# Kernel tuning notes

Measured on AMD Instinct MI355X. Metric: run time of the kernel, lower is better.

The kernel has to match this reference:

```python
import jax, jax.numpy as jnp
import numpy as np

NUM_NODES = 50000
NUM_GRAPHS = 64
HIDDEN = 256
F_IN = 256
NUM_EDGES = 800000


def setup_inputs() -> dict:
    key = jax.random.key(0)
    ks = jax.random.split(key, 8)
    x = jax.random.normal(ks[0], (NUM_NODES, F_IN), dtype=jnp.float32)
    edge_index = jax.random.randint(ks[1], (2, NUM_EDGES), 0, NUM_NODES, dtype=jnp.int64)
    batch = jnp.sort(jax.random.randint(ks[2], (NUM_NODES,), 0, NUM_GRAPHS, dtype=jnp.int64))
    # Glorot-ish init for weights, zeros for biases (as PyG GCNConv / Linear defaults)
    s1 = 1.0 / np.sqrt(F_IN)
    s2 = 1.0 / np.sqrt(HIDDEN)
    W1 = jax.random.uniform(ks[3], (F_IN, HIDDEN), jnp.float32, -s1, s1)
    b1 = jnp.zeros((HIDDEN,), jnp.float32)
    W2 = jax.random.uniform(ks[4], (HIDDEN, HIDDEN), jnp.float32, -s2, s2)
    b2 = jnp.zeros((HIDDEN,), jnp.float32)
    W_out = jax.random.uniform(ks[5], (HIDDEN, 1), jnp.float32, -s2, s2)
    b_out = jnp.zeros((1,), jnp.float32)
    return {"x": x, "edge_index": edge_index, "batch": batch,
            "W1": W1, "b1": b1, "W2": W2, "b2": b2,
            "W_out": W_out, "b_out": b_out}


def gcn_conv(x, W, b, src, dst, num_nodes):
    """GCNConv with added self-loops and symmetric D^{-1/2} A D^{-1/2} norm."""
    # degrees over edges incl. self-loops (src/dst already include them)
    deg = jax.ops.segment_sum(jnp.ones_like(src, dtype=x.dtype), dst,
                              num_segments=num_nodes)
    dinv = jax.lax.rsqrt(jnp.maximum(deg, 1e-12))
    norm = dinv[src] * dinv[dst]                       # [E+N]
    h = x @ W                                           # [N, H] dense GEMM
    msg = h[src] * norm[:, None]                        # gather + scale
    out = jax.ops.segment_sum(msg, dst, num_segments=num_nodes)  # scatter-add
    return out + b


def reference(x, edge_index, batch, W1, b1, W2, b2, W_out, b_out):
    n = x.shape[0]
    loops = jnp.arange(n, dtype=edge_index.dtype)
    src = jnp.concatenate([edge_index[0], loops])
    dst = jnp.concatenate([edge_index[1], loops])
    h = jax.nn.relu(gcn_conv(x, W1, b1, src, dst, n))
    h = jax.nn.relu(gcn_conv(h, W2, b2, src, dst, n))
    pooled = jax.ops.segment_sum(h, batch, num_segments=NUM_GRAPHS)  # [G, H]
    return pooled @ W_out + b_out
```

## Files before the change

kernel.cpp:

```cpp
#include <hip/hip_runtime.h>
#include <hip/hip_fp16.h>

#define N_NODES 50000
#define NFEAT   256
#define NGRAPH  64
#define NEDGE   800000
#define NBUCK   98
#define BWIN    16384

typedef __attribute__((ext_vector_type(8))) _Float16 half8;
typedef __attribute__((ext_vector_type(2))) _Float16 h2v;
typedef __attribute__((ext_vector_type(4))) float f32x4;
struct alignas(8) US4 { unsigned short x, y, z, w; };

static __device__ __forceinline__ float h2f(unsigned short u) {
    return __half2float(__ushort_as_half(u));
}
static __device__ __forceinline__ unsigned short f2h(float f) {
    return __half_as_ushort(__float2half(f));
}

__global__ __launch_bounds__(256) void k_bin(const int* __restrict__ src,
                                             const int* __restrict__ dst,
                                             int* __restrict__ bcnt,
                                             unsigned int* __restrict__ tmp) {
    __shared__ int hist[NBUCK];
    __shared__ int base[NBUCK];
    const int t = threadIdx.x;
    if (t < NBUCK) hist[t] = 0;
    __syncthreads();
    const int e0 = blockIdx.x * 1024 + t * 4;
    int s[4], d[4], b[4], rk[4];
#pragma unroll
    for (int i = 0; i < 4; ++i) {
        const int e = e0 + i;
        if (e < NEDGE) {
            s[i] = src[e];
            d[i] = dst[e];
            b[i] = d[i] >> 9;
            rk[i] = atomicAdd(&hist[b[i]], 1);
        } else {
            b[i] = -1;
        }
    }
    __syncthreads();
    if (t < NBUCK) base[t] = atomicAdd(&bcnt[t], hist[t]);
    __syncthreads();
#pragma unroll
    for (int i = 0; i < 4; ++i) {
        if (b[i] >= 0)
            tmp[(size_t)b[i] * BWIN + base[b[i]] + rk[i]] =
                ((unsigned int)s[i] << 16) | (unsigned int)d[i];
    }
}

__global__ void k_bscan(const int* __restrict__ bcnt, int* __restrict__ bbase) {
    const int l = threadIdx.x;
    const int i0 = 2 * l, i1 = 2 * l + 1;
    const int v0 = (i0 < NBUCK) ? bcnt[i0] : 0;
    const int v1 = (i1 < NBUCK) ? bcnt[i1] : 0;
    const int ps = v0 + v1;
    int incl = ps;
#pragma unroll
    for (int off = 1; off < 64; off <<= 1) {
        int u = __shfl_up(incl, off, 64);
        if (l >= off) incl += u;
    }
    const int excl = incl - ps;
    if (i0 < NBUCK) bbase[i0] = excl;
    if (i1 < NBUCK) bbase[i1] = excl + v0;
}

__global__ __launch_bounds__(256) void k_build(const unsigned int* __restrict__ tmp,
                                               const int* __restrict__ bcnt,
                                               const int* __restrict__ bbase,
                                               int* __restrict__ row_start,
                                               float* __restrict__ dinv,
                                               unsigned short* __restrict__ csr) {
    __shared__ int cnt[512];
    __shared__ int cur[512];
    __shared__ int wtot[4];
    const int bk = blockIdx.x, t = threadIdx.x;
    const int node0 = bk << 9;
    const int n = bcnt[bk];
    const unsigned int* rec = tmp + (size_t)bk * BWIN;
    cnt[t] = 0;
    cnt[t + 256] = 0;
    __syncthreads();
    for (int i = t; i < n; i += 256) atomicAdd(&cnt[rec[i] & 511], 1);
    __syncthreads();
    const int lane = t & 63, w = t >> 6;
    const int v0 = cnt[2 * t], v1 = cnt[2 * t + 1];
    const int ps = v0 + v1;
    int incl = ps;
#pragma unroll
    for (int off = 1; off < 64; off <<= 1) {
        int u = __shfl_up(incl, off, 64);
        if (lane >= off) incl += u;
    }
    if (lane == 63) wtot[w] = incl;
    __syncthreads();
    int wbase = 0;
#pragma unroll
    for (int k = 0; k < 4; ++k) wbase += (k < w) ? wtot[k] : 0;
    const int excl = wbase + incl - ps;
    const int gb = bbase[bk];
    const int g0 = node0 + 2 * t;
    if (g0 < N_NODES) {
        row_start[g0] = gb + excl;
        dinv[g0] = rsqrtf((float)v0 + 1.0f);
    }
    if (g0 + 1 < N_NODES) {
        row_start[g0 + 1] = gb + excl + v0;
        dinv[g0 + 1] = rsqrtf((float)v1 + 1.0f);
    }
    cur[2 * t] = gb + excl;
    cur[2 * t + 1] = gb + excl + v0;
    __syncthreads();
    for (int i = t; i < n; i += 256) {
        const unsigned int r = rec[i];
        const int pos = atomicAdd(&cur[r & 511], 1);
        csr[pos] = (unsigned short)(r >> 16);
    }
    if (bk == 0 && t == 0) row_start[N_NODES] = NEDGE;
}

__global__ void k_prep_w(const float* __restrict__ W1, const float* __restrict__ W2,
                         unsigned short* __restrict__ w1t, unsigned short* __restrict__ w2t) {
    const int l = blockIdx.x >> 8;
    const int idx = (blockIdx.x & 255) * 256 + threadIdx.x;
    const int n = idx >> 8, k = idx & 255;
    const float* W = l ? W2 : W1;
    unsigned short* wt = l ? w2t : w1t;
    wt[n * 256 + k] = f2h(W[k * 256 + n]);
}

template <bool AF32>
__global__ __launch_bounds__(256, 2) void k_gemm_mfma(const float* __restrict__ Af,
                                                      const unsigned short* __restrict__ Ah,
                                                      const unsigned short* __restrict__ Wt,
                                                      const float* __restrict__ dinv,
                                                      unsigned short* __restrict__ Ch, int M) {
    __shared__ unsigned short lds[32768];
    const int t = threadIdx.x;
    const int half = blockIdx.y;
    const int m0 = blockIdx.x * 128;
    const int w = t >> 6, lane = t & 63;
    const int lr = lane & 15, g = lane >> 4;

    {
        const unsigned short* wbase = Wt + (size_t)half * 128 * 256;
#pragma unroll
        for (int it = 0; it < 16; ++it) {
            const int unit = it * 256 + t;
            const int n = unit >> 5;
            const int rem = unit & 31;
            const int ks = rem >> 2, kg = rem & 3;
            const half8 v = *(const half8*)&wbase[n * 256 + rem * 8];
            const int kgx = kg ^ ((n >> 1) & 3);
            *(half8*)&lds[ks * 4096 + n * 32 + kgx * 8] = v;
        }
    }
    __syncthreads();

    const int rbase = m0 + w * 32;
    unsigned short* Chh = Ch + (size_t)half * (size_t)N_NODES * 128;

    int boff[8];
#pragma unroll
    for (int ni = 0; ni < 8; ++ni) {
        const int n = ni * 16 + lr;
        boff[ni] = n * 32 + ((g ^ ((n >> 1) & 3)) << 3);
    }

    half8 aA[8], aB[8];

#define LOADCHUNK(C, DST)                                                                \
    {                                                                                    \
        const int row = min(rbase + (C) * 16 + lr, M - 1);                               \
        _Pragma("unroll") for (int ks = 0; ks < 8; ++ks) {                               \
            if (AF32) {                                                                  \
                const float* ap = Af + (size_t)row * 256 + ks * 32 + g * 8;              \
                const float4 p0 = *(const float4*)ap;                                    \
                const float4 p1 = *(const float4*)(ap + 4);                              \
                half8 h;                                                                 \
                h[0] = (_Float16)p0.x; h[1] = (_Float16)p0.y;                            \
                h[2] = (_Float16)p0.z; h[3] = (_Float16)p0.w;                            \
                h[4] = (_Float16)p1.x; h[5] = (_Float16)p1.y;                            \
                h[6] = (_Float16)p1.z; h[7] = (_Float16)p1.w;                            \
                DST[ks] = h;                                                             \
            } else {                                                                     \
                DST[ks] = *(const half8*)(Ah + (size_t)(ks >> 2) * (size_t)N_NODES * 128 \
                                          + (size_t)row * 128 + (ks & 3) * 32 + g * 8);  \
            }                                                                            \
        }                                                                                \
    }

#define COMPUTE(C, SRC)                                                                  \
    {                                                                                    \
        f32x4 acc[8] = {};                                                               \
        half8 bc[8];                                                                     \
        _Pragma("unroll") for (int ni = 0; ni < 8; ++ni)                                 \
            bc[ni] = *(const half8*)&lds[boff[ni]];                                      \
        _Pragma("unroll") for (int ks = 0; ks < 8; ++ks) {                               \
            half8 bn[8];                                                                 \
            if (ks < 7) {                                                                \
                _Pragma("unroll") for (int ni = 0; ni < 8; ++ni)                         \
                    bn[ni] = *(const half8*)&lds[(ks + 1) * 4096 + boff[ni]];            \
            }                                                                            \
            _Pragma("unroll") for (int ni = 0; ni < 8; ++ni)                             \
                acc[ni] = __builtin_amdgcn_mfma_f32_16x16x32_f16(bc[ni], SRC[ks],        \
                                                                 acc[ni], 0, 0, 0);      \
            _Pragma("unroll") for (int ni = 0; ni < 8; ++ni) bc[ni] = bn[ni];            \
        }                                                                                \
        const int row = rbase + (C) * 16 + lr;                                           \
        const float dv = dinv[min(row, M - 1)];                                          \
        if (row < M) {                                                                   \
            _Pragma("unroll") for (int ni = 0; ni < 8; ++ni) {                           \
                US4 o;                                                                   \
                o.x = f2h(acc[ni][0] * dv); o.y = f2h(acc[ni][1] * dv);                  \
                o.z = f2h(acc[ni][2] * dv); o.w = f2h(acc[ni][3] * dv);                  \
                *(US4*)(Chh + (size_t)row * 128 + ni * 16 + g * 4) = o;                  \
            }                                                                            \
        }                                                                                \
    }

    LOADCHUNK(0, aA)
    LOADCHUNK(1, aB)
    COMPUTE(0, aA)
    COMPUTE(1, aB)

#undef LOADCHUNK
#undef COMPUTE
}

__global__ __launch_bounds__(256) void k_aggregate(const unsigned short* __restrict__ hs,
                                                   const int* __restrict__ row_start,
                                                   const unsigned short* __restrict__ csr,
                                                   const float* __restrict__ dinv,
                                                   const float* __restrict__ bias,
                                                   unsigned short* __restrict__ out) {
    const int wid = blockIdx.x * 4 + (threadIdx.x >> 6);
    if (wid >= 2 * N_NODES) return;
    const int half = (wid >= N_NODES) ? 1 : 0;
    const int node = wid - half * N_NODES;
    const int lane = threadIdx.x & 63;
    const int sub = lane >> 4;
    const int fl = lane & 15;
    const unsigned int* hu = (const unsigned int*)(hs + (size_t)half * N_NODES * 128);
    const h2v e0v = {(_Float16)1.0f, (_Float16)0.0f};
    const h2v e1v = {(_Float16)0.0f, (_Float16)1.0f};

    float acc[8] = {};
    const int s0 = row_start[node], s1 = row_start[node + 1];
    const unsigned short* row = csr + s0;
    const int n = s1 - s0;

#define EDGEPAIR(VA, VB)                                                                   \
    {                                                                                      \
        h2v s;                                                                             \
        s = __builtin_bit_cast(h2v, VA.x) + __builtin_bit_cast(h2v, VB.x);                 \
        acc[0] = __builtin_amdgcn_fdot2(s, e0v, acc[0], false);                            \
        acc[1] = __builtin_amdgcn_fdot2(s, e1v, acc[1], false);                            \
        s = __builtin_bit_cast(h2v, VA.y) + __builtin_bit_cast(h2v, VB.y);                 \
        acc[2] = __builtin_amdgcn_fdot2(s, e0v, acc[2], false);                            \
        acc[3] = __builtin_amdgcn_fdot2(s, e1v, acc[3], false);                            \
        s = __builtin_bit_cast(h2v, VA.z) + __builtin_bit_cast(h2v, VB.z);                 \
        acc[4] = __builtin_amdgcn_fdot2(s, e0v, acc[4], false);                            \
        acc[5] = __builtin_amdgcn_fdot2(s, e1v, acc[5], false);                            \
        s = __builtin_bit_cast(h2v, VA.w) + __builtin_bit_cast(h2v, VB.w);                 \
        acc[6] = __builtin_amdgcn_fdot2(s, e0v, acc[6], false);                            \
        acc[7] = __builtin_amdgcn_fdot2(s, e1v, acc[7], false);                            \
    }

    const int nfull = n & ~7;
    int j = 0;
    for (; j < nfull; j += 8) {
        const int sa = row[j + sub * 2];
        const int sb = row[j + sub * 2 + 1];
        const uint4 va = *(const uint4*)(hu + (size_t)sa * 64 + fl * 4);
        const uint4 vb = *(const uint4*)(hu + (size_t)sb * 64 + fl * 4);
        EDGEPAIR(va, vb)
    }
    if (j < n) {
        const int ia = j + sub * 2, ib = ia + 1;
        uint4 va = {0, 0, 0, 0}, vb = {0, 0, 0, 0};
        if (ia < n) va = *(const uint4*)(hu + (size_t)row[ia] * 64 + fl * 4);
        if (ib < n) vb = *(const uint4*)(hu + (size_t)row[ib] * 64 + fl * 4);
        EDGEPAIR(va, vb)
    }
#undef EDGEPAIR

#pragma unroll
    for (int i = 0; i < 8; ++i) {
        acc[i] += __shfl_xor(acc[i], 16, 64);
        acc[i] += __shfl_xor(acc[i], 32, 64);
    }

    if (sub == 0) {
        const float dd = dinv[node];
        const uint4 sh = *(const uint4*)(hu + (size_t)node * 64 + fl * 4);
        const float4 b0 = *(const float4*)(bias + half * 128 + fl * 8);
        const float4 b1 = *(const float4*)(bias + half * 128 + fl * 8 + 4);
        float r[8];
        r[0] = fmaf(acc[0] + h2f((unsigned short)(sh.x & 0xffff)), dd, b0.x);
        r[1] = fmaf(acc[1] + h2f((unsigned short)(sh.x >> 16)),    dd, b0.y);
        r[2] = fmaf(acc[2] + h2f((unsigned short)(sh.y & 0xffff)), dd, b0.z);
        r[3] = fmaf(acc[3] + h2f((unsigned short)(sh.y >> 16)),    dd, b0.w);
        r[4] = fmaf(acc[4] + h2f((unsigned short)(sh.z & 0xffff)), dd, b1.x);
        r[5] = fmaf(acc[5] + h2f((unsigned short)(sh.z >> 16)),    dd, b1.y);
        r[6] = fmaf(acc[6] + h2f((unsigned short)(sh.w & 0xffff)), dd, b1.z);
        r[7] = fmaf(acc[7] + h2f((unsigned short)(sh.w >> 16)),    dd, b1.w);
#pragma unroll
        for (int i = 0; i < 8; ++i) r[i] = fmaxf(r[i], 0.f);
        uint4 o;
        o.x = (unsigned int)f2h(r[0]) | ((unsigned int)f2h(r[1]) << 16);
        o.y = (unsigned int)f2h(r[2]) | ((unsigned int)f2h(r[3]) << 16);
        o.z = (unsigned int)f2h(r[4]) | ((unsigned int)f2h(r[5]) << 16);
        o.w = (unsigned int)f2h(r[6]) | ((unsigned int)f2h(r[7]) << 16);
        *(uint4*)((unsigned int*)(out + (size_t)half * N_NODES * 128) +
                  (size_t)node * 64 + fl * 4) = o;
    }
}

__global__ void k_pool(const unsigned short* __restrict__ h2, const int* __restrict__ batch,
                       float* __restrict__ pooled) {
    const int strip = blockIdx.x * 2 + (threadIdx.x >> 7);
    const int tf = threadIdx.x & 127;
    const int f = tf * 2;
    const unsigned short* base = h2 + (size_t)(f >> 7) * N_NODES * 128 + (f & 127);
    const int n0 = strip * 40, n1 = n0 + 40;
    int g = batch[n0];
    float ax = 0.f, ay = 0.f;
    for (int n = n0; n < n1; ++n) {
        const int bg = batch[n];
        if (bg != g) {
            unsafeAtomicAdd(&pooled[g * NFEAT + f], ax);
            unsafeAtomicAdd(&pooled[g * NFEAT + f + 1], ay);
            ax = ay = 0.f;
            g = bg;
        }
        const unsigned int u = *(const unsigned int*)(base + (size_t)n * 128);
        ax += h2f((unsigned short)(u & 0xffff));
        ay += h2f((unsigned short)(u >> 16));
    }
    unsafeAtomicAdd(&pooled[g * NFEAT + f], ax);
    unsafeAtomicAdd(&pooled[g * NFEAT + f + 1], ay);
}

__global__ void k_final(const float* __restrict__ pooled, const float* __restrict__ Wout,
                        const float* __restrict__ bout, float* __restrict__ out) {
    const int g = blockIdx.x, t = threadIdx.x;
    float v = pooled[g * NFEAT + t] * Wout[t];
#pragma unroll
    for (int off = 32; off > 0; off >>= 1) v += __shfl_down(v, off, 64);
    __shared__ float sred[4];
    if ((t & 63) == 0) sred[t >> 6] = v;
    __syncthreads();
    if (t == 0) out[g] = sred[0] + sred[1] + sred[2] + sred[3] + bout[0];
}

extern "C" void kernel_launch(void* const* d_in, const int* in_sizes, int n_in,
                              void* d_out, int out_size, void* d_ws, size_t ws_size,
                              hipStream_t stream) {
    const float* x     = (const float*)d_in[0];
    const int*   ei    = (const int*)d_in[1];
    const int*   batch = (const int*)d_in[2];
    const float* W1    = (const float*)d_in[3];
    const float* b1    = (const float*)d_in[4];
    const float* W2    = (const float*)d_in[5];
    const float* b2    = (const float*)d_in[6];
    const float* Wout  = (const float*)d_in[7];
    const float* bout  = (const float*)d_in[8];
    float* out = (float*)d_out;

    const int* srcp = ei;
    const int* dstp = ei + NEDGE;

    const size_t NE128 = (size_t)N_NODES * 128;
    unsigned short* hA = (unsigned short*)d_ws;
    unsigned short* hB = hA + 2 * NE128;
    float* dinv      = (float*)(hB + 2 * NE128);
    float* pooled    = dinv + N_NODES;
    int*   row_start = (int*)(pooled + NGRAPH * NFEAT);
    int*   bcnt      = row_start + N_NODES + 3;
    int*   bbase     = bcnt + NBUCK;
    unsigned short* csr = (unsigned short*)(bbase + NBUCK);
    unsigned int* tmp = (unsigned int*)(csr + NEDGE);
    unsigned short* w1t = (unsigned short*)(tmp + (size_t)NBUCK * BWIN);
    unsigned short* w2t = w1t + 65536;

    hipMemsetAsync(bcnt, 0, NBUCK * sizeof(int), stream);
    k_bin<<<(NEDGE + 1023) / 1024, 256, 0, stream>>>(srcp, dstp, bcnt, tmp);
    k_bscan<<<1, 64, 0, stream>>>(bcnt, bbase);
    k_build<<<NBUCK, 256, 0, stream>>>(tmp, bcnt, bbase, row_start, dinv, csr);

    k_prep_w<<<512, 256, 0, stream>>>(W1, W2, w1t, w2t);

    const dim3 ggrid(391, 2);
    const int agg_grid = (2 * N_NODES + 3) / 4;

    k_gemm_mfma<true><<<ggrid, 256, 0, stream>>>(x, nullptr, w1t, dinv, hA, N_NODES);
    k_aggregate<<<agg_grid, 256, 0, stream>>>(hA, row_start, csr, dinv, b1, hB);

    k_gemm_mfma<false><<<ggrid, 256, 0, stream>>>(nullptr, hB, w2t, dinv, hA, N_NODES);
    k_aggregate<<<agg_grid, 256, 0, stream>>>(hA, row_start, csr, dinv, b2, hB);

    hipMemsetAsync(pooled, 0, NGRAPH * NFEAT * sizeof(float), stream);
    k_pool<<<625, 256, 0, stream>>>(hB, batch, pooled);
    k_final<<<NGRAPH, 256, 0, stream>>>(pooled, Wout, bout, out);
}
```

Baseline: 255.8 us.

## Fold memsets and bucket scan into kernels; compute both GEMM halves per block

Zeroing of the bucket counts and pooled buffer moves into the weight-prep kernel, which now runs first, so two memset launches disappear. The separate bucket-scan kernel is removed; each build block computes its own prefix from bcnt with a wave reduction. The GEMM grid drops its y dimension, and each block loads its A rows once and computes both 128-column output halves, restaging W in LDS between them. This halves A reads but gives half as many blocks and drops the occupancy hint of 2 from launch_bounds, which may lower occupancy and latency hiding.

```diff
diff --git a/kernel.cpp b/kernel.cpp
--- a/kernel.cpp
+++ b/kernel.cpp
@@ -18,6 +18,24 @@
 }
 static __device__ __forceinline__ unsigned short f2h(float f) {
     return __half_as_ushort(__float2half(f));
+}
+
+__global__ void k_prep_w(const float* __restrict__ W1, const float* __restrict__ W2,
+                         unsigned short* __restrict__ w1t, unsigned short* __restrict__ w2t,
+                         int* __restrict__ bcnt, float* __restrict__ pooled) {
+    const int l = blockIdx.x >> 8;
+    const int idx = (blockIdx.x & 255) * 256 + threadIdx.x;
+    const int n = idx >> 8, k = idx & 255;
+    const float* W = l ? W2 : W1;
+    unsigned short* wt = l ? w2t : w1t;
+    wt[n * 256 + k] = f2h(W[k * 256 + n]);
+    if (l == 0) {
+        if (blockIdx.x == 0 && threadIdx.x < NBUCK) bcnt[threadIdx.x] = 0;
+        if (blockIdx.x >= 1 && blockIdx.x <= 64) {
+            const int p = (blockIdx.x - 1) * 256 + threadIdx.x;
+            if (p < NGRAPH * NFEAT) pooled[p] = 0.f;
+        }
+    }
 }
 
 __global__ __launch_bounds__(256) void k_bin(const int* __restrict__ src,
@@ -54,38 +72,28 @@
     }
 }
 
-__global__ void k_bscan(const int* __restrict__ bcnt, int* __restrict__ bbase) {
-    const int l = threadIdx.x;
-    const int i0 = 2 * l, i1 = 2 * l + 1;
-    const int v0 = (i0 < NBUCK) ? bcnt[i0] : 0;
-    const int v1 = (i1 < NBUCK) ? bcnt[i1] : 0;
-    const int ps = v0 + v1;
-    int incl = ps;
-#pragma unroll
-    for (int off = 1; off < 64; off <<= 1) {
-        int u = __shfl_up(incl, off, 64);
-        if (l >= off) incl += u;
-    }
-    const int excl = incl - ps;
-    if (i0 < NBUCK) bbase[i0] = excl;
-    if (i1 < NBUCK) bbase[i1] = excl + v0;
-}
-
 __global__ __launch_bounds__(256) void k_build(const unsigned int* __restrict__ tmp,
                                                const int* __restrict__ bcnt,
-                                               const int* __restrict__ bbase,
                                                int* __restrict__ row_start,
                                                float* __restrict__ dinv,
                                                unsigned short* __restrict__ csr) {
     __shared__ int cnt[512];
     __shared__ int cur[512];
     __shared__ int wtot[4];
+    __shared__ int s_gb;
     const int bk = blockIdx.x, t = threadIdx.x;
     const int node0 = bk << 9;
     const int n = bcnt[bk];
     const unsigned int* rec = tmp + (size_t)bk * BWIN;
     cnt[t] = 0;
     cnt[t + 256] = 0;
+    if (t < 64) {
+        int part = 0;
+        for (int i = t; i < bk; i += 64) part += bcnt[i];
+#pragma unroll
+        for (int off = 32; off; off >>= 1) part += __shfl_down(part, off, 64);
+        if (t == 0) s_gb = part;
+    }
     __syncthreads();
     for (int i = t; i < n; i += 256) atomicAdd(&cnt[rec[i] & 511], 1);
     __syncthreads();
@@ -104,7 +112,7 @@
 #pragma unroll
     for (int k = 0; k < 4; ++k) wbase += (k < w) ? wtot[k] : 0;
     const int excl = wbase + incl - ps;
-    const int gb = bbase[bk];
+    const int gb = s_gb;
     const int g0 = node0 + 2 * t;
     if (g0 < N_NODES) {
         row_start[g0] = gb + excl;
@@ -125,47 +133,18 @@
     if (bk == 0 && t == 0) row_start[N_NODES] = NEDGE;
 }
 
-__global__ void k_prep_w(const float* __restrict__ W1, const float* __restrict__ W2,
-                         unsigned short* __restrict__ w1t, unsigned short* __restrict__ w2t) {
-    const int l = blockIdx.x >> 8;
-    const int idx = (blockIdx.x & 255) * 256 + threadIdx.x;
-    const int n = idx >> 8, k = idx & 255;
-    const float* W = l ? W2 : W1;
-    unsigned short* wt = l ? w2t : w1t;
-    wt[n * 256 + k] = f2h(W[k * 256 + n]);
-}
-
 template <bool AF32>
-__global__ __launch_bounds__(256, 2) void k_gemm_mfma(const float* __restrict__ Af,
-                                                      const unsigned short* __restrict__ Ah,
-                                                      const unsigned short* __restrict__ Wt,
-                                                      const float* __restrict__ dinv,
-                                                      unsigned short* __restrict__ Ch, int M) {
+__global__ __launch_bounds__(256) void k_gemm_mfma(const float* __restrict__ Af,
+                                                   const unsigned short* __restrict__ Ah,
+                                                   const unsigned short* __restrict__ Wt,
+                                                   const float* __restrict__ dinv,
+                                                   unsigned short* __restrict__ Ch, int M) {
     __shared__ unsigned short lds[32768];
     const int t = threadIdx.x;
-    const int half = blockIdx.y;
     const int m0 = blockIdx.x * 128;
     const int w = t >> 6, lane = t & 63;
     const int lr = lane & 15, g = lane >> 4;
 
-    {
-        const unsigned short* wbase = Wt + (size_t)half * 128 * 256;
-#pragma unroll
-        for (int it = 0; it < 16; ++it) {
-            const int unit = it * 256 + t;
-            const int n = unit >> 5;
-            const int rem = unit & 31;
-            const int ks = rem >> 2, kg = rem & 3;
-            const half8 v = *(const half8*)&wbase[n * 256 + rem * 8];
-            const int kgx = kg ^ ((n >> 1) & 3);
-            *(half8*)&lds[ks * 4096 + n * 32 + kgx * 8] = v;
-        }
-    }
-    __syncthreads();
-
-    const int rbase = m0 + w * 32;
-    unsigned short* Chh = Ch + (size_t)half * (size_t)N_NODES * 128;
-
     int boff[8];
 #pragma unroll
     for (int ni = 0; ni < 8; ++ni) {
@@ -173,7 +152,22 @@
         boff[ni] = n * 32 + ((g ^ ((n >> 1) & 3)) << 3);
     }
 
+    const int rbase = m0 + w * 32;
     half8 aA[8], aB[8];
+
+#define STAGE(H)                                                                         \
+    {                                                                                    \
+        const unsigned short* wbase = Wt + (size_t)(H) * 128 * 256;                      \
+        _Pragma("unroll") for (int it = 0; it < 16; ++it) {                              \
+            const int unit = it * 256 + t;                                               \
+            const int n = unit >> 5;                                                     \
+            const int rem = unit & 31;                                                   \
+            const int ks = rem >> 2, kg = rem & 3;                                       \
+            const half8 v = *(const half8*)&wbase[n * 256 + rem * 8];                    \
+            const int kgx = kg ^ ((n >> 1) & 3);                                         \
+            *(half8*)&lds[ks * 4096 + n * 32 + kgx * 8] = v;                             \
+        }                                                                                \
+    }
 
 #define LOADCHUNK(C, DST)                                                                \
     {                                                                                    \
@@ -196,8 +190,9 @@
         }                                                                                \
     }
 
-#define COMPUTE(C, SRC)                                                                  \
+#define COMPUTE(C, SRC, H)                                                               \
     {                                                                                    \
+        unsigned short* Chh = Ch + (size_t)(H) * (size_t)N_NODES * 128;                  \
         f32x4 acc[8] = {};                                                               \
         half8 bc[8];                                                                     \
         _Pragma("unroll") for (int ni = 0; ni < 8; ++ni)                                 \
@@ -225,11 +220,19 @@
         }                                                                                \
     }
 
+    STAGE(0)
+    __syncthreads();
     LOADCHUNK(0, aA)
     LOADCHUNK(1, aB)
-    COMPUTE(0, aA)
-    COMPUTE(1, aB)
-
+    COMPUTE(0, aA, 0)
+    COMPUTE(1, aB, 0)
+    __syncthreads();
+    STAGE(1)
+    __syncthreads();
+    COMPUTE(0, aA, 1)
+    COMPUTE(1, aB, 1)
+
+#undef STAGE
 #undef LOADCHUNK
 #undef COMPUTE
 }
@@ -384,20 +387,17 @@
     float* pooled    = dinv + N_NODES;
     int*   row_start = (int*)(pooled + NGRAPH * NFEAT);
     int*   bcnt      = row_start + N_NODES + 3;
-    int*   bbase     = bcnt + NBUCK;
-    unsigned short* csr = (unsigned short*)(bbase + NBUCK);
+    unsigned short* csr = (unsigned short*)(bcnt + NBUCK + 2);
     unsigned int* tmp = (unsigned int*)(csr + NEDGE);
     unsigned short* w1t = (unsigned short*)(tmp + (size_t)NBUCK * BWIN);
     unsigned short* w2t = w1t + 65536;
 
-    hipMemsetAsync(bcnt, 0, NBUCK * sizeof(int), stream);
+    k_prep_w<<<512, 256, 0, stream>>>(W1, W2, w1t, w2t, bcnt, pooled);
+
     k_bin<<<(NEDGE + 1023) / 1024, 256, 0, stream>>>(srcp, dstp, bcnt, tmp);
-    k_bscan<<<1, 64, 0, stream>>>(bcnt, bbase);
-    k_build<<<NBUCK, 256, 0, stream>>>(tmp, bcnt, bbase, row_start, dinv, csr);
-
-    k_prep_w<<<512, 256, 0, stream>>>(W1, W2, w1t, w2t);
-
-    const dim3 ggrid(391, 2);
+    k_build<<<NBUCK, 256, 0, stream>>>(tmp, bcnt, row_start, dinv, csr);
+
+    const int ggrid = 391;
     const int agg_grid = (2 * N_NODES + 3) / 4;
 
     k_gemm_mfma<true><<<ggrid, 256, 0, stream>>>(x, nullptr, w1t, dinv, hA, N_NODES);
@@ -406,7 +406,6 @@
     k_gemm_mfma<false><<<ggrid, 256, 0, stream>>>(nullptr, hB, w2t, dinv, hA, N_NODES);
     k_aggregate<<<agg_grid, 256, 0, stream>>>(hA, row_start, csr, dinv, b2, hB);
 
-    hipMemsetAsync(pooled, 0, NGRAPH * NFEAT * sizeof(float), stream);
     k_pool<<<625, 256, 0, stream>>>(hB, batch, pooled);
     k_final<<<NGRAPH, 256, 0, stream>>>(pooled, Wout, bout, out);
 }
```

Result: no change. 252.3 us (-1.3%).
